# Optimization experiments

Hardware: AMD Instinct MI355X
Metric: run time of the kernel (lower is better)

Reference implementation:

```python
import jax, jax.numpy as jnp
import numpy as np

N, K, F, W = 32768, 32, 4, 256

def setup_inputs() -> dict:
    key = jax.random.key(0)
    ks = jax.random.split(key, 12)
    init = lambda k, shape, fan_in: jax.random.normal(k, shape, jnp.float32) / np.sqrt(fan_in)
    return {
        "h_center": jax.random.normal(ks[0], (N, W), jnp.float32),
        "h_neighbors": jax.random.normal(ks[1], (N, K, W), jnp.float32),
        "differences": jax.random.normal(ks[2], (N, K, F), jnp.float32),
        # filter MLP (depth=2): Dense(W) -> silu -> Dense(W)
        "W_f1": init(ks[3], (F, W), F),
        "b_f1": jnp.zeros((W,), jnp.float32),
        "W_f2": init(ks[4], (W, W), W),
        "b_f2": jnp.zeros((W,), jnp.float32),
        # neighbor projection Dense(W)
        "W_nb": init(ks[5], (W, W), W),
        "b_nb": jnp.zeros((W,), jnp.float32),
        # center projection Dense(W)
        "W_c": init(ks[6], (W, W), W),
        "b_c": jnp.zeros((W,), jnp.float32),
    }

def reference(h_center, h_neighbors, differences, W_f1, b_f1, W_f2, b_f2, W_nb, b_nb, W_c, b_c):
    # filter MLP over edge (difference) features: [N,K,F] -> [N,K,W]
    f = jax.nn.silu(differences @ W_f1 + b_f1)
    filter_kernel = f @ W_f2 + b_f2
    # project neighbor features: [N,K,W]
    h_nb = h_neighbors @ W_nb + b_nb
    # gated message, sum over neighbor axis -> [N,W]
    msg = jnp.sum(filter_kernel * h_nb, axis=-2)
    # center dense + message, silu
    h_out = jax.nn.silu(h_center @ W_c + b_c + msg)
    return h_out
```

## Files before the change

kernel.cpp:

```cpp
#include <hip/hip_runtime.h>
#include <hip/hip_bf16.h>
#include <stdint.h>

#define NN 32768
#define KNBR 32
#define FDIM 4
#define WDIM 256

typedef __attribute__((ext_vector_type(8))) short short8;
typedef __attribute__((ext_vector_type(4))) float f32x4;

__device__ __forceinline__ unsigned int f2bf(float x) {
    union { float f; unsigned int u; } c; c.f = x;
    return (c.u + 0x7FFFu + ((c.u >> 16) & 1u)) >> 16;
}
__device__ __forceinline__ unsigned int pk2(float a, float b) {
    return f2bf(a) | (f2bf(b) << 16);
}
__device__ __forceinline__ float silu_f(float x) {
    return x / (1.0f + __expf(-x));
}

__global__ void prep_weights(const float* __restrict__ Wf2,
                             const float* __restrict__ Wnb,
                             const float* __restrict__ Wc,
                             uint4* __restrict__ ws_out) {
    int t = blockIdx.x * 256 + threadIdx.x;
    int w = t >> 13;
    int q = t & 8191;
    int kt = q >> 10;
    int nt = (q >> 6) & 15;
    int lane = q & 63;
    int k0 = kt * 32 + ((lane >> 4) << 3);
    int col = nt * 16 + (lane & 15);
    const float* src = (w == 0) ? Wf2 : (w == 1) ? Wnb : Wc;
    const float* p = src + (size_t)k0 * 256 + col;
    uint4 o;
    o.x = pk2(p[0],        p[256]);
    o.y = pk2(p[512],      p[768]);
    o.z = pk2(p[1024],     p[1280]);
    o.w = pk2(p[1536],     p[1792]);
    ws_out[t] = o;
}

__global__ __launch_bounds__(512) void msg_kernel(
        const float* __restrict__ nbr,
        const float* __restrict__ diff,
        const float* __restrict__ Wf1,
        const float* __restrict__ b1,
        const float* __restrict__ b2,
        const float* __restrict__ bnb,
        const uint4* __restrict__ wf2_g,
        const uint4* __restrict__ wnb_g,
        float* __restrict__ msg_out)
{
    __shared__ unsigned short f_frag[8 * 8 * 64 * 8];
    __shared__ unsigned short e_frag[8 * 2 * 64 * 8];
    __shared__ unsigned short wnb_s[2 * 16 * 64 * 8];
    __shared__ unsigned short wf2_s[2 * 16 * 64 * 8];
    __shared__ float wf1_s[4 * 256];
    __shared__ float b1_s[256];

    const int tid  = threadIdx.x;
    const int lane = tid & 63;
    const int wid  = tid >> 6;
    const int wm   = wid >> 2;
    const int wn   = wid & 3;
    const int eblk = blockIdx.x * 128;

    for (int i = tid; i < 1024; i += 512) wf1_s[i] = Wf1[i];
    if (tid < 256) b1_s[tid] = b1[tid];
    __syncthreads();

    uint4* ff4 = (uint4*)f_frag;
    #pragma unroll
    for (int j = 0; j < 8; ++j) {
        int q   = tid + j * 512;
        int lq  = q & 63;
        int ktf = (q >> 6) & 7;
        int mt  = q >> 9;
        int row = mt * 16 + (lq & 15);
        int k0  = ktf * 32 + ((lq >> 4) << 3);
        const float4 d4 = *(const float4*)(diff + (size_t)(eblk + row) * 4);
        float vals[8];
        #pragma unroll
        for (int i = 0; i < 8; ++i) {
            int k = k0 + i;
            float v = b1_s[k] + d4.x * wf1_s[k]       + d4.y * wf1_s[256 + k]
                              + d4.z * wf1_s[512 + k] + d4.w * wf1_s[768 + k];
            vals[i] = silu_f(v);
        }
        uint4 o;
        o.x = pk2(vals[0], vals[1]); o.y = pk2(vals[2], vals[3]);
        o.z = pk2(vals[4], vals[5]); o.w = pk2(vals[6], vals[7]);
        ff4[q] = o;
    }
    __syncthreads();

    f32x4 accH[4][4], accP[4][4];
    #pragma unroll
    for (int mt = 0; mt < 4; ++mt)
        #pragma unroll
        for (int nt = 0; nt < 4; ++nt) {
            accH[mt][nt] = (f32x4){0.f, 0.f, 0.f, 0.f};
            accP[mt][nt] = (f32x4){0.f, 0.f, 0.f, 0.f};
        }

    uint4* ef4 = (uint4*)e_frag;
    for (int kt2 = 0; kt2 < 4; ++kt2) {
        {
            int row = tid >> 2, quarter = tid & 3;
            const float* src = nbr + (size_t)(eblk + row) * 256 + kt2 * 64 + quarter * 16;
            float4 v0 = *(const float4*)(src + 0);
            float4 v1 = *(const float4*)(src + 4);
            float4 v2 = *(const float4*)(src + 8);
            float4 v3 = *(const float4*)(src + 12);
            uint4 p0, p1;
            p0.x = pk2(v0.x, v0.y); p0.y = pk2(v0.z, v0.w);
            p0.z = pk2(v1.x, v1.y); p0.w = pk2(v1.z, v1.w);
            p1.x = pk2(v2.x, v2.y); p1.y = pk2(v2.z, v2.w);
            p1.z = pk2(v3.x, v3.y); p1.w = pk2(v3.z, v3.w);
            int mt = row >> 4, kti = quarter >> 1, fr = row & 15;
            int g0 = (quarter & 1) * 2;
            ef4[(mt * 2 + kti) * 64 + g0 * 16 + fr]       = p0;
            ef4[(mt * 2 + kti) * 64 + (g0 + 1) * 16 + fr] = p1;
        }
        {
            const uint4* srcn = wnb_g + kt2 * 2048;
            const uint4* srcf = wf2_g + kt2 * 2048;
            uint4* dn = (uint4*)wnb_s;
            uint4* df = (uint4*)wf2_s;
            #pragma unroll
            for (int j = 0; j < 4; ++j) {
                dn[j * 512 + tid] = srcn[j * 512 + tid];
                df[j * 512 + tid] = srcf[j * 512 + tid];
            }
        }
        __syncthreads();

        #pragma unroll
        for (int kti = 0; kti < 2; ++kti) {
            short8 bN[4], bF[4];
            #pragma unroll
            for (int nt = 0; nt < 4; ++nt) {
                int ntg = wn * 4 + nt;
                bN[nt] = *(const short8*)&wnb_s[((kti * 16 + ntg) * 64 + lane) * 8];
                bF[nt] = *(const short8*)&wf2_s[((kti * 16 + ntg) * 64 + lane) * 8];
            }
            #pragma unroll
            for (int mt = 0; mt < 4; ++mt) {
                int mtg = wm * 4 + mt;
                short8 aE = *(const short8*)&e_frag[((mtg * 2 + kti) * 64 + lane) * 8];
                short8 aF = *(const short8*)&f_frag[((mtg * 8 + kt2 * 2 + kti) * 64 + lane) * 8];
                #pragma unroll
                for (int nt = 0; nt < 4; ++nt) {
                    accH[mt][nt] = __builtin_amdgcn_mfma_f32_16x16x32_bf16(aE, bN[nt], accH[mt][nt], 0, 0, 0);
                    accP[mt][nt] = __builtin_amdgcn_mfma_f32_16x16x32_bf16(aF, bF[nt], accP[mt][nt], 0, 0, 0);
                }
            }
        }
        __syncthreads();
    }

    #pragma unroll
    for (int nd = 0; nd < 2; ++nd) {
        int node = blockIdx.x * 4 + wm * 2 + nd;
        #pragma unroll
        for (int nt = 0; nt < 4; ++nt) {
            int col = wn * 64 + nt * 16 + (lane & 15);
            float vb2 = b2[col];
            float vbn = bnb[col];
            float s = 0.f;
            #pragma unroll
            for (int m2 = 0; m2 < 2; ++m2) {
                int mt = nd * 2 + m2;
                #pragma unroll
                for (int r = 0; r < 4; ++r)
                    s += (accP[mt][nt][r] + vb2) * (accH[mt][nt][r] + vbn);
            }
            s += __shfl_xor(s, 16);
            s += __shfl_xor(s, 32);
            if (lane < 16) msg_out[(size_t)node * 256 + col] = s;
        }
    }
}

__global__ __launch_bounds__(256) void out_kernel(
        const float* __restrict__ hc,
        const float* __restrict__ bc,
        const uint4* __restrict__ wc_g,
        float* __restrict__ out)
{
    __shared__ unsigned short a_s[4 * 2 * 64 * 8];
    __shared__ unsigned short wc_s[2 * 16 * 64 * 8];

    const int tid  = threadIdx.x;
    const int lane = tid & 63;
    const int wn   = tid >> 6;
    const int rblk = blockIdx.x * 64;

    f32x4 acc[4][4];
    #pragma unroll
    for (int mt = 0; mt < 4; ++mt)
        #pragma unroll
        for (int nt = 0; nt < 4; ++nt)
            acc[mt][nt] = (f32x4){0.f, 0.f, 0.f, 0.f};

    uint4* af4 = (uint4*)a_s;
    for (int kt2 = 0; kt2 < 4; ++kt2) {
        {
            int row = tid >> 2, quarter = tid & 3;
            const float* src = hc + (size_t)(rblk + row) * 256 + kt2 * 64 + quarter * 16;
            float4 v0 = *(const float4*)(src + 0);
            float4 v1 = *(const float4*)(src + 4);
            float4 v2 = *(const float4*)(src + 8);
            float4 v3 = *(const float4*)(src + 12);
            uint4 p0, p1;
            p0.x = pk2(v0.x, v0.y); p0.y = pk2(v0.z, v0.w);
            p0.z = pk2(v1.x, v1.y); p0.w = pk2(v1.z, v1.w);
            p1.x = pk2(v2.x, v2.y); p1.y = pk2(v2.z, v2.w);
            p1.z = pk2(v3.x, v3.y); p1.w = pk2(v3.z, v3.w);
            int mt = row >> 4, kti = quarter >> 1, fr = row & 15;
            int g0 = (quarter & 1) * 2;
            af4[(mt * 2 + kti) * 64 + g0 * 16 + fr]       = p0;
            af4[(mt * 2 + kti) * 64 + (g0 + 1) * 16 + fr] = p1;
            const uint4* srcw = wc_g + kt2 * 2048;
            uint4* dw = (uint4*)wc_s;
            #pragma unroll
            for (int j = 0; j < 8; ++j)
                dw[j * 256 + tid] = srcw[j * 256 + tid];
        }
        __syncthreads();
        #pragma unroll
        for (int kti = 0; kti < 2; ++kti) {
            short8 b[4];
            #pragma unroll
            for (int nt = 0; nt < 4; ++nt)
                b[nt] = *(const short8*)&wc_s[((kti * 16 + wn * 4 + nt) * 64 + lane) * 8];
            #pragma unroll
            for (int mt = 0; mt < 4; ++mt) {
                short8 a = *(const short8*)&a_s[((mt * 2 + kti) * 64 + lane) * 8];
                #pragma unroll
                for (int nt = 0; nt < 4; ++nt)
                    acc[mt][nt] = __builtin_amdgcn_mfma_f32_16x16x32_bf16(a, b[nt], acc[mt][nt], 0, 0, 0);
            }
        }
        __syncthreads();
    }

    #pragma unroll
    for (int mt = 0; mt < 4; ++mt)
        #pragma unroll
        for (int nt = 0; nt < 4; ++nt)
            #pragma unroll
            for (int r = 0; r < 4; ++r) {
                int grow = rblk + mt * 16 + ((lane >> 4) << 2) + r;
                int col  = wn * 64 + nt * 16 + (lane & 15);
                size_t idx = (size_t)grow * 256 + col;
                float v = acc[mt][nt][r] + bc[col] + out[idx];
                out[idx] = silu_f(v);
            }
}

extern "C" void kernel_launch(void* const* d_in, const int* in_sizes, int n_in,
                              void* d_out, int out_size, void* d_ws, size_t ws_size,
                              hipStream_t stream) {
    const float* h_center    = (const float*)d_in[0];
    const float* h_neighbors = (const float*)d_in[1];
    const float* differences = (const float*)d_in[2];
    const float* W_f1        = (const float*)d_in[3];
    const float* b_f1        = (const float*)d_in[4];
    const float* W_f2        = (const float*)d_in[5];
    const float* b_f2        = (const float*)d_in[6];
    const float* W_nb        = (const float*)d_in[7];
    const float* b_nb        = (const float*)d_in[8];
    const float* W_c         = (const float*)d_in[9];
    const float* b_c         = (const float*)d_in[10];
    float* out = (float*)d_out;

    uint4* ws4 = (uint4*)d_ws;
    const uint4* wf2_ws = ws4;
    const uint4* wnb_ws = ws4 + 8192;
    const uint4* wc_ws  = ws4 + 16384;

    prep_weights<<<96, 256, 0, stream>>>(W_f2, W_nb, W_c, ws4);
    msg_kernel<<<NN / 4, 512, 0, stream>>>(h_neighbors, differences, W_f1, b_f1,
                                           b_f2, b_nb, wf2_ws, wnb_ws, out);
    out_kernel<<<NN / 64, 256, 0, stream>>>(h_center, b_c, wc_ws, out);
}
```

Before: 713.2 us.

## Split msg kernel into two sequential GEMM phases to cut registers and LDS

Restructures msg_kernel so each block handles 64 edges (2 nodes) and runs the filter GEMM and neighbor-projection GEMM sequentially rather than interleaved. The filter result is stashed in LDS as bf16 (phi_s), which halves the accumulators per wave and drops the large f_frag buffer. Launch bounds now request 4 blocks per CU for higher occupancy. The cost is twice as many blocks, extra barriers, weight tiles reloaded per block for half the edges, and an additional bf16 rounding of the filter output.

```diff
diff --git a/kernel.cpp b/kernel.cpp
--- a/kernel.cpp
+++ b/kernel.cpp
@@ -43,7 +43,7 @@
     ws_out[t] = o;
 }
 
-__global__ __launch_bounds__(512) void msg_kernel(
+__global__ __launch_bounds__(512, 4) void msg_kernel(
         const float* __restrict__ nbr,
         const float* __restrict__ diff,
         const float* __restrict__ Wf1,
@@ -54,109 +54,114 @@
         const uint4* __restrict__ wnb_g,
         float* __restrict__ msg_out)
 {
-    __shared__ unsigned short f_frag[8 * 8 * 64 * 8];
-    __shared__ unsigned short e_frag[8 * 2 * 64 * 8];
-    __shared__ unsigned short wnb_s[2 * 16 * 64 * 8];
-    __shared__ unsigned short wf2_s[2 * 16 * 64 * 8];
-    __shared__ float wf1_s[4 * 256];
+    __shared__ unsigned short stage_s[8 * 64 * 8];
+    __shared__ unsigned short w_s[2 * 16 * 64 * 8];
+    __shared__ unsigned int   phi_s[8192];
+    __shared__ float wf1_s[1024];
     __shared__ float b1_s[256];
 
     const int tid  = threadIdx.x;
     const int lane = tid & 63;
     const int wid  = tid >> 6;
-    const int wm   = wid >> 2;
-    const int wn   = wid & 3;
-    const int eblk = blockIdx.x * 128;
+    const int eblk = blockIdx.x * 64;
+
+    const int g    = wid;
+    const int row  = ((g >> 1) << 4) + (lane & 15);
+    const int klo  = ((g & 1) << 5) + ((lane >> 4) << 3);
 
     for (int i = tid; i < 1024; i += 512) wf1_s[i] = Wf1[i];
     if (tid < 256) b1_s[tid] = b1[tid];
+    const float4 d4 = *(const float4*)(diff + (size_t)(eblk + row) * 4);
+
+    uint4* stage4 = (uint4*)stage_s;
+    uint4* ws4l   = (uint4*)w_s;
+
+    f32x4 acc[4][2];
+    #pragma unroll
+    for (int mt = 0; mt < 4; ++mt) {
+        acc[mt][0] = (f32x4){0.f, 0.f, 0.f, 0.f};
+        acc[mt][1] = (f32x4){0.f, 0.f, 0.f, 0.f};
+    }
+
     __syncthreads();
 
-    uint4* ff4 = (uint4*)f_frag;
-    #pragma unroll
-    for (int j = 0; j < 8; ++j) {
-        int q   = tid + j * 512;
-        int lq  = q & 63;
-        int ktf = (q >> 6) & 7;
-        int mt  = q >> 9;
-        int row = mt * 16 + (lq & 15);
-        int k0  = ktf * 32 + ((lq >> 4) << 3);
-        const float4 d4 = *(const float4*)(diff + (size_t)(eblk + row) * 4);
-        float vals[8];
-        #pragma unroll
-        for (int i = 0; i < 8; ++i) {
-            int k = k0 + i;
-            float v = b1_s[k] + d4.x * wf1_s[k]       + d4.y * wf1_s[256 + k]
-                              + d4.z * wf1_s[512 + k] + d4.w * wf1_s[768 + k];
-            vals[i] = silu_f(v);
-        }
-        uint4 o;
-        o.x = pk2(vals[0], vals[1]); o.y = pk2(vals[2], vals[3]);
-        o.z = pk2(vals[4], vals[5]); o.w = pk2(vals[6], vals[7]);
-        ff4[q] = o;
-    }
-    __syncthreads();
-
-    f32x4 accH[4][4], accP[4][4];
-    #pragma unroll
-    for (int mt = 0; mt < 4; ++mt)
-        #pragma unroll
-        for (int nt = 0; nt < 4; ++nt) {
-            accH[mt][nt] = (f32x4){0.f, 0.f, 0.f, 0.f};
-            accP[mt][nt] = (f32x4){0.f, 0.f, 0.f, 0.f};
-        }
-
-    uint4* ef4 = (uint4*)e_frag;
     for (int kt2 = 0; kt2 < 4; ++kt2) {
         {
-            int row = tid >> 2, quarter = tid & 3;
-            const float* src = nbr + (size_t)(eblk + row) * 256 + kt2 * 64 + quarter * 16;
-            float4 v0 = *(const float4*)(src + 0);
+            const int kb = kt2 * 64 + klo;
+            float vals[8];
+            #pragma unroll
+            for (int i = 0; i < 8; ++i) {
+                int k = kb + i;
+                float v = b1_s[k] + d4.x * wf1_s[k]       + d4.y * wf1_s[256 + k]
+                                  + d4.z * wf1_s[512 + k] + d4.w * wf1_s[768 + k];
+                vals[i] = silu_f(v);
+            }
+            uint4 o;
+            o.x = pk2(vals[0], vals[1]); o.y = pk2(vals[2], vals[3]);
+            o.z = pk2(vals[4], vals[5]); o.w = pk2(vals[6], vals[7]);
+            stage4[tid] = o;
+        }
+        {
+            const uint4* srcw = wf2_g + (size_t)kt2 * 2048;
+            ws4l[tid]        = srcw[tid];
+            ws4l[512 + tid]  = srcw[512 + tid];
+            ws4l[1024 + tid] = srcw[1024 + tid];
+            ws4l[1536 + tid] = srcw[1536 + tid];
+        }
+        __syncthreads();
+        #pragma unroll
+        for (int kti = 0; kti < 2; ++kti) {
+            short8 bA = *(const short8*)&w_s[((kti * 16 + wid * 2 + 0) * 64 + lane) * 8];
+            short8 bB = *(const short8*)&w_s[((kti * 16 + wid * 2 + 1) * 64 + lane) * 8];
+            #pragma unroll
+            for (int mt = 0; mt < 4; ++mt) {
+                short8 a = *(const short8*)&stage_s[((mt * 2 + kti) * 64 + lane) * 8];
+                acc[mt][0] = __builtin_amdgcn_mfma_f32_16x16x32_bf16(a, bA, acc[mt][0], 0, 0, 0);
+                acc[mt][1] = __builtin_amdgcn_mfma_f32_16x16x32_bf16(a, bB, acc[mt][1], 0, 0, 0);
+            }
+        }
+        __syncthreads();
+    }
+
+    #pragma unroll
+    for (int nt = 0; nt < 2; ++nt) {
+        float vb2 = b2[wid * 32 + nt * 16 + (lane & 15)];
+        #pragma unroll
+        for (int mt = 0; mt < 4; ++mt) {
+            int base = (((wid * 2 + nt) * 4 + mt) * 64 + lane) * 2;
+            phi_s[base]     = pk2(acc[mt][nt][0] + vb2, acc[mt][nt][1] + vb2);
+            phi_s[base + 1] = pk2(acc[mt][nt][2] + vb2, acc[mt][nt][3] + vb2);
+            acc[mt][nt] = (f32x4){0.f, 0.f, 0.f, 0.f};
+        }
+    }
+
+    for (int kt2 = 0; kt2 < 4; ++kt2) {
+        {
+            const float* src = nbr + (size_t)(eblk + row) * 256 + kt2 * 64 + klo;
+            float4 v0 = *(const float4*)(src);
             float4 v1 = *(const float4*)(src + 4);
-            float4 v2 = *(const float4*)(src + 8);
-            float4 v3 = *(const float4*)(src + 12);
-            uint4 p0, p1;
-            p0.x = pk2(v0.x, v0.y); p0.y = pk2(v0.z, v0.w);
-            p0.z = pk2(v1.x, v1.y); p0.w = pk2(v1.z, v1.w);
-            p1.x = pk2(v2.x, v2.y); p1.y = pk2(v2.z, v2.w);
-            p1.z = pk2(v3.x, v3.y); p1.w = pk2(v3.z, v3.w);
-            int mt = row >> 4, kti = quarter >> 1, fr = row & 15;
-            int g0 = (quarter & 1) * 2;
-            ef4[(mt * 2 + kti) * 64 + g0 * 16 + fr]       = p0;
-            ef4[(mt * 2 + kti) * 64 + (g0 + 1) * 16 + fr] = p1;
-        }
-        {
-            const uint4* srcn = wnb_g + kt2 * 2048;
-            const uint4* srcf = wf2_g + kt2 * 2048;
-            uint4* dn = (uint4*)wnb_s;
-            uint4* df = (uint4*)wf2_s;
-            #pragma unroll
-            for (int j = 0; j < 4; ++j) {
-                dn[j * 512 + tid] = srcn[j * 512 + tid];
-                df[j * 512 + tid] = srcf[j * 512 + tid];
-            }
-        }
-        __syncthreads();
-
+            uint4 o;
+            o.x = pk2(v0.x, v0.y); o.y = pk2(v0.z, v0.w);
+            o.z = pk2(v1.x, v1.y); o.w = pk2(v1.z, v1.w);
+            stage4[tid] = o;
+        }
+        {
+            const uint4* srcw = wnb_g + (size_t)kt2 * 2048;
+            ws4l[tid]        = srcw[tid];
+            ws4l[512 + tid]  = srcw[512 + tid];
+            ws4l[1024 + tid] = srcw[1024 + tid];
+            ws4l[1536 + tid] = srcw[1536 + tid];
+        }
+        __syncthreads();
         #pragma unroll
         for (int kti = 0; kti < 2; ++kti) {
-            short8 bN[4], bF[4];
-            #pragma unroll
-            for (int nt = 0; nt < 4; ++nt) {
-                int ntg = wn * 4 + nt;
-                bN[nt] = *(const short8*)&wnb_s[((kti * 16 + ntg) * 64 + lane) * 8];
-                bF[nt] = *(const short8*)&wf2_s[((kti * 16 + ntg) * 64 + lane) * 8];
-            }
+            short8 bA = *(const short8*)&w_s[((kti * 16 + wid * 2 + 0) * 64 + lane) * 8];
+            short8 bB = *(const short8*)&w_s[((kti * 16 + wid * 2 + 1) * 64 + lane) * 8];
             #pragma unroll
             for (int mt = 0; mt < 4; ++mt) {
-                int mtg = wm * 4 + mt;
-                short8 aE = *(const short8*)&e_frag[((mtg * 2 + kti) * 64 + lane) * 8];
-                short8 aF = *(const short8*)&f_frag[((mtg * 8 + kt2 * 2 + kti) * 64 + lane) * 8];
-                #pragma unroll
-                for (int nt = 0; nt < 4; ++nt) {
-                    accH[mt][nt] = __builtin_amdgcn_mfma_f32_16x16x32_bf16(aE, bN[nt], accH[mt][nt], 0, 0, 0);
-                    accP[mt][nt] = __builtin_amdgcn_mfma_f32_16x16x32_bf16(aF, bF[nt], accP[mt][nt], 0, 0, 0);
-                }
+                short8 a = *(const short8*)&stage_s[((mt * 2 + kti) * 64 + lane) * 8];
+                acc[mt][0] = __builtin_amdgcn_mfma_f32_16x16x32_bf16(a, bA, acc[mt][0], 0, 0, 0);
+                acc[mt][1] = __builtin_amdgcn_mfma_f32_16x16x32_bf16(a, bB, acc[mt][1], 0, 0, 0);
             }
         }
         __syncthreads();
@@ -164,19 +169,23 @@
 
     #pragma unroll
     for (int nd = 0; nd < 2; ++nd) {
-        int node = blockIdx.x * 4 + wm * 2 + nd;
-        #pragma unroll
-        for (int nt = 0; nt < 4; ++nt) {
-            int col = wn * 64 + nt * 16 + (lane & 15);
-            float vb2 = b2[col];
-            float vbn = bnb[col];
+        int node = blockIdx.x * 2 + nd;
+        #pragma unroll
+        for (int nt = 0; nt < 2; ++nt) {
+            int col = wid * 32 + nt * 16 + (lane & 15);
+            float bn = bnb[col];
             float s = 0.f;
             #pragma unroll
             for (int m2 = 0; m2 < 2; ++m2) {
                 int mt = nd * 2 + m2;
-                #pragma unroll
-                for (int r = 0; r < 4; ++r)
-                    s += (accP[mt][nt][r] + vb2) * (accH[mt][nt][r] + vbn);
+                int base = (((wid * 2 + nt) * 4 + mt) * 64 + lane) * 2;
+                unsigned int p01 = phi_s[base], p23 = phi_s[base + 1];
+                float ph0 = __uint_as_float(p01 << 16);
+                float ph1 = __uint_as_float(p01 & 0xffff0000u);
+                float ph2 = __uint_as_float(p23 << 16);
+                float ph3 = __uint_as_float(p23 & 0xffff0000u);
+                s += ph0 * (acc[mt][nt][0] + bn) + ph1 * (acc[mt][nt][1] + bn)
+                   + ph2 * (acc[mt][nt][2] + bn) + ph3 * (acc[mt][nt][3] + bn);
             }
             s += __shfl_xor(s, 16);
             s += __shfl_xor(s, 32);
@@ -284,7 +293,7 @@
     const uint4* wc_ws  = ws4 + 16384;
 
     prep_weights<<<96, 256, 0, stream>>>(W_f2, W_nb, W_c, ws4);
-    msg_kernel<<<NN / 4, 512, 0, stream>>>(h_neighbors, differences, W_f1, b_f1,
+    msg_kernel<<<NN / 2, 512, 0, stream>>>(h_neighbors, differences, W_f1, b_f1,
                                            b_f2, b_nb, wf2_ws, wnb_ws, out);
     out_kernel<<<NN / 64, 256, 0, stream>>>(h_center, b_c, wc_ws, out);
 }
```

New measurement: 640.0 us. 1.11x faster.

## Make msg kernel persistent over tiles with register-resident weights and double buffering

Applied to the files above, without the earlier changes.

Rewrites the message kernel so that each block processes 8 tiles of 64 edges. The W_f2 and W_nb fragments are loaded once into registers per wave, instead of being restaged through shared memory on every k-step. The next tile's neighbor and difference loads are issued before the current tile's MFMAs, and the converted fragments are written to a double-buffered LDS slot, so global latency overlaps with compute. A cheaper round-to-nearest bf16 pack is also used. The large register footprint (64 short8 weight fragments) with launch_bounds(512,2) risks spilling or low occupancy.

```diff
diff --git a/kernel.cpp b/kernel.cpp
--- a/kernel.cpp
+++ b/kernel.cpp
@@ -6,6 +6,7 @@
 #define KNBR 32
 #define FDIM 4
 #define WDIM 256
+#define TPB_TILES 8
 
 typedef __attribute__((ext_vector_type(8))) short short8;
 typedef __attribute__((ext_vector_type(4))) float f32x4;
@@ -16,6 +17,11 @@
 }
 __device__ __forceinline__ unsigned int pk2(float a, float b) {
     return f2bf(a) | (f2bf(b) << 16);
+}
+__device__ __forceinline__ unsigned int pkr(float a, float b) {
+    unsigned ua = __float_as_uint(a) + 0x8000u;
+    unsigned ub = __float_as_uint(b) + 0x8000u;
+    return (ua >> 16) | (ub & 0xFFFF0000u);
 }
 __device__ __forceinline__ float silu_f(float x) {
     return x / (1.0f + __expf(-x));
@@ -43,7 +49,7 @@
     ws_out[t] = o;
 }
 
-__global__ __launch_bounds__(512) void msg_kernel(
+__global__ __launch_bounds__(512, 2) void msg_kernel(
         const float* __restrict__ nbr,
         const float* __restrict__ diff,
         const float* __restrict__ Wf1,
@@ -54,134 +60,178 @@
         const uint4* __restrict__ wnb_g,
         float* __restrict__ msg_out)
 {
-    __shared__ unsigned short f_frag[8 * 8 * 64 * 8];
-    __shared__ unsigned short e_frag[8 * 2 * 64 * 8];
-    __shared__ unsigned short wnb_s[2 * 16 * 64 * 8];
-    __shared__ unsigned short wf2_s[2 * 16 * 64 * 8];
-    __shared__ float wf1_s[4 * 256];
+    __shared__ uint4 fbuf[2][2048];
+    __shared__ uint4 ebuf[2][2048];
+    __shared__ float wf1_s[1024];
     __shared__ float b1_s[256];
 
     const int tid  = threadIdx.x;
     const int lane = tid & 63;
     const int wid  = tid >> 6;
-    const int wm   = wid >> 2;
-    const int wn   = wid & 3;
-    const int eblk = blockIdx.x * 128;
+    const int srow = tid >> 3;
+    const int skti = tid & 7;
+    const int smt  = srow >> 4;
+    const int sfr  = srow & 15;
+    const int mtf  = lane >> 4;
+    const int frf  = lane & 15;
 
     for (int i = tid; i < 1024; i += 512) wf1_s[i] = Wf1[i];
     if (tid < 256) b1_s[tid] = b1[tid];
+
+    const short8* wf2p = (const short8*)wf2_g;
+    const short8* wnbp = (const short8*)wnb_g;
+    short8 bF[8][2], bN[8][2];
+    #pragma unroll
+    for (int kti = 0; kti < 8; ++kti) {
+        #pragma unroll
+        for (int nt = 0; nt < 2; ++nt) {
+            const int idx = (kti * 16 + wid * 2 + nt) * 64 + lane;
+            bF[kti][nt] = wf2p[idx];
+            bN[kti][nt] = wnbp[idx];
+        }
+    }
+    float vb2[2], vbn[2];
+    #pragma unroll
+    for (int nt = 0; nt < 2; ++nt) {
+        const int col = wid * 32 + nt * 16 + frf;
+        vb2[nt] = b2[col];
+        vbn[nt] = bnb[col];
+    }
+
+    f32x4 accP[4][2], accH[4][2];
+    #pragma unroll
+    for (int mt = 0; mt < 4; ++mt)
+        #pragma unroll
+        for (int nt = 0; nt < 2; ++nt) {
+            accP[mt][nt] = (f32x4){0.f,0.f,0.f,0.f};
+            accH[mt][nt] = (f32x4){0.f,0.f,0.f,0.f};
+        }
+
+    const int tbase = blockIdx.x * TPB_TILES;
+
+    auto stage_f = [&](int bsel, float4 d4) {
+        uint4* fb = fbuf[bsel];
+        const float4* w4 = (const float4*)wf1_s;
+        const float4* b4 = (const float4*)b1_s;
+        #pragma unroll
+        for (int g = 0; g < 4; ++g) {
+            const int o = wid * 8 + g * 2;
+            float4 ba = b4[o],      bb = b4[o+1];
+            float4 w0a = w4[o],     w0b = w4[o+1];
+            float4 w1a = w4[64+o],  w1b = w4[64+o+1];
+            float4 w2a = w4[128+o], w2b = w4[128+o+1];
+            float4 w3a = w4[192+o], w3b = w4[192+o+1];
+            float v0 = silu_f(ba.x + d4.x*w0a.x + d4.y*w1a.x + d4.z*w2a.x + d4.w*w3a.x);
+            float v1 = silu_f(ba.y + d4.x*w0a.y + d4.y*w1a.y + d4.z*w2a.y + d4.w*w3a.y);
+            float v2 = silu_f(ba.z + d4.x*w0a.z + d4.y*w1a.z + d4.z*w2a.z + d4.w*w3a.z);
+            float v3 = silu_f(ba.w + d4.x*w0a.w + d4.y*w1a.w + d4.z*w2a.w + d4.w*w3a.w);
+            float v4 = silu_f(bb.x + d4.x*w0b.x + d4.y*w1b.x + d4.z*w2b.x + d4.w*w3b.x);
+            float v5 = silu_f(bb.y + d4.x*w0b.y + d4.y*w1b.y + d4.z*w2b.y + d4.w*w3b.y);
+            float v6 = silu_f(bb.z + d4.x*w0b.z + d4.y*w1b.z + d4.z*w2b.z + d4.w*w3b.z);
+            float v7 = silu_f(bb.w + d4.x*w0b.w + d4.y*w1b.w + d4.z*w2b.w + d4.w*w3b.w);
+            uint4 o4;
+            o4.x = pkr(v0, v1); o4.y = pkr(v2, v3);
+            o4.z = pkr(v4, v5); o4.w = pkr(v6, v7);
+            fb[(mtf * 8 + wid) * 64 + g * 16 + frf] = o4;
+        }
+    };
+    auto stage_e = [&](int bsel, const float4* evA, const float4* evB) {
+        uint4* eb = ebuf[bsel];
+        #pragma unroll
+        for (int g = 0; g < 2; ++g) {
+            float4 a = evA[g*2], b = evA[g*2+1];
+            uint4 o4;
+            o4.x = pkr(a.x,a.y); o4.y = pkr(a.z,a.w);
+            o4.z = pkr(b.x,b.y); o4.w = pkr(b.z,b.w);
+            eb[(smt * 8 + skti) * 64 + g * 16 + sfr] = o4;
+        }
+        #pragma unroll
+        for (int g = 2; g < 4; ++g) {
+            float4 a = evB[(g-2)*2], b = evB[(g-2)*2+1];
+            uint4 o4;
+            o4.x = pkr(a.x,a.y); o4.y = pkr(a.z,a.w);
+            o4.z = pkr(b.x,b.y); o4.w = pkr(b.z,b.w);
+            eb[(smt * 8 + skti) * 64 + g * 16 + sfr] = o4;
+        }
+    };
+
     __syncthreads();
 
-    uint4* ff4 = (uint4*)f_frag;
-    #pragma unroll
-    for (int j = 0; j < 8; ++j) {
-        int q   = tid + j * 512;
-        int lq  = q & 63;
-        int ktf = (q >> 6) & 7;
-        int mt  = q >> 9;
-        int row = mt * 16 + (lq & 15);
-        int k0  = ktf * 32 + ((lq >> 4) << 3);
-        const float4 d4 = *(const float4*)(diff + (size_t)(eblk + row) * 4);
-        float vals[8];
-        #pragma unroll
-        for (int i = 0; i < 8; ++i) {
-            int k = k0 + i;
-            float v = b1_s[k] + d4.x * wf1_s[k]       + d4.y * wf1_s[256 + k]
-                              + d4.z * wf1_s[512 + k] + d4.w * wf1_s[768 + k];
-            vals[i] = silu_f(v);
-        }
-        uint4 o;
-        o.x = pk2(vals[0], vals[1]); o.y = pk2(vals[2], vals[3]);
-        o.z = pk2(vals[4], vals[5]); o.w = pk2(vals[6], vals[7]);
-        ff4[q] = o;
+    {
+        const int eblk = tbase * 64;
+        float4 d4 = *(const float4*)(diff + (size_t)(eblk + lane) * 4);
+        const float4* ep = (const float4*)(nbr + (size_t)(eblk + srow) * 256 + skti * 32);
+        float4 evA[4] = {ep[0], ep[1], ep[2], ep[3]};
+        float4 evB[4] = {ep[4], ep[5], ep[6], ep[7]};
+        stage_e(0, evA, evB);
+        stage_f(0, d4);
     }
     __syncthreads();
 
-    f32x4 accH[4][4], accP[4][4];
-    #pragma unroll
-    for (int mt = 0; mt < 4; ++mt)
-        #pragma unroll
-        for (int nt = 0; nt < 4; ++nt) {
-            accH[mt][nt] = (f32x4){0.f, 0.f, 0.f, 0.f};
-            accP[mt][nt] = (f32x4){0.f, 0.f, 0.f, 0.f};
-        }
-
-    uint4* ef4 = (uint4*)e_frag;
-    for (int kt2 = 0; kt2 < 4; ++kt2) {
+    for (int t = 0; t < TPB_TILES; ++t) {
+        const int cur = t & 1;
+        const bool more = (t + 1 < TPB_TILES);
+
+        float4 d4n = (float4){0.f,0.f,0.f,0.f};
+        float4 evA[4], evB[4];
+        if (more) {
+            const int eblk = (tbase + t + 1) * 64;
+            d4n = *(const float4*)(diff + (size_t)(eblk + lane) * 4);
+            const float4* epn = (const float4*)(nbr + (size_t)(eblk + srow) * 256 + skti * 32);
+            evA[0] = epn[0]; evA[1] = epn[1]; evA[2] = epn[2]; evA[3] = epn[3];
+            evB[0] = epn[4]; evB[1] = epn[5]; evB[2] = epn[6]; evB[3] = epn[7];
+        }
+
         {
-            int row = tid >> 2, quarter = tid & 3;
-            const float* src = nbr + (size_t)(eblk + row) * 256 + kt2 * 64 + quarter * 16;
-            float4 v0 = *(const float4*)(src + 0);
-            float4 v1 = *(const float4*)(src + 4);
-            float4 v2 = *(const float4*)(src + 8);
-            float4 v3 = *(const float4*)(src + 12);
-            uint4 p0, p1;
-            p0.x = pk2(v0.x, v0.y); p0.y = pk2(v0.z, v0.w);
-            p0.z = pk2(v1.x, v1.y); p0.w = pk2(v1.z, v1.w);
-            p1.x = pk2(v2.x, v2.y); p1.y = pk2(v2.z, v2.w);
-            p1.z = pk2(v3.x, v3.y); p1.w = pk2(v3.z, v3.w);
-            int mt = row >> 4, kti = quarter >> 1, fr = row & 15;
-            int g0 = (quarter & 1) * 2;
-            ef4[(mt * 2 + kti) * 64 + g0 * 16 + fr]       = p0;
-            ef4[(mt * 2 + kti) * 64 + (g0 + 1) * 16 + fr] = p1;
-        }
-        {
-            const uint4* srcn = wnb_g + kt2 * 2048;
-            const uint4* srcf = wf2_g + kt2 * 2048;
-            uint4* dn = (uint4*)wnb_s;
-            uint4* df = (uint4*)wf2_s;
-            #pragma unroll
-            for (int j = 0; j < 4; ++j) {
-                dn[j * 512 + tid] = srcn[j * 512 + tid];
-                df[j * 512 + tid] = srcf[j * 512 + tid];
-            }
-        }
+            const short8* fb = (const short8*)fbuf[cur];
+            const short8* eb = (const short8*)ebuf[cur];
+            #pragma unroll
+            for (int kti = 0; kti < 8; ++kti) {
+                #pragma unroll
+                for (int mt = 0; mt < 4; ++mt) {
+                    short8 aF = fb[(mt * 8 + kti) * 64 + lane];
+                    short8 aE = eb[(mt * 8 + kti) * 64 + lane];
+                    accP[mt][0] = __builtin_amdgcn_mfma_f32_16x16x32_bf16(aF, bF[kti][0], accP[mt][0], 0, 0, 0);
+                    accP[mt][1] = __builtin_amdgcn_mfma_f32_16x16x32_bf16(aF, bF[kti][1], accP[mt][1], 0, 0, 0);
+                    accH[mt][0] = __builtin_amdgcn_mfma_f32_16x16x32_bf16(aE, bN[kti][0], accH[mt][0], 0, 0, 0);
+                    accH[mt][1] = __builtin_amdgcn_mfma_f32_16x16x32_bf16(aE, bN[kti][1], accH[mt][1], 0, 0, 0);
+                }
+            }
+        }
+
+        if (more) {
+            stage_e(1 - cur, evA, evB);
+            stage_f(1 - cur, d4n);
+        }
+
+        const int nodeBase = (tbase + t) * 2;
+        #pragma unroll
+        for (int nd = 0; nd < 2; ++nd) {
+            #pragma unroll
+            for (int nt = 0; nt < 2; ++nt) {
+                float s = 0.f;
+                #pragma unroll
+                for (int m2 = 0; m2 < 2; ++m2) {
+                    const int mt = nd * 2 + m2;
+                    #pragma unroll
+                    for (int r = 0; r < 4; ++r)
+                        s += (accP[mt][nt][r] + vb2[nt]) * (accH[mt][nt][r] + vbn[nt]);
+                }
+                s += __shfl_xor(s, 16);
+                s += __shfl_xor(s, 32);
+                if (lane < 16)
+                    msg_out[(size_t)(nodeBase + nd) * 256 + wid * 32 + nt * 16 + lane] = s;
+            }
+        }
+        #pragma unroll
+        for (int mt = 0; mt < 4; ++mt)
+            #pragma unroll
+            for (int nt = 0; nt < 2; ++nt) {
+                accP[mt][nt] = (f32x4){0.f,0.f,0.f,0.f};
+                accH[mt][nt] = (f32x4){0.f,0.f,0.f,0.f};
+            }
+
         __syncthreads();
-
-        #pragma unroll
-        for (int kti = 0; kti < 2; ++kti) {
-            short8 bN[4], bF[4];
-            #pragma unroll
-            for (int nt = 0; nt < 4; ++nt) {
-                int ntg = wn * 4 + nt;
-                bN[nt] = *(const short8*)&wnb_s[((kti * 16 + ntg) * 64 + lane) * 8];
-                bF[nt] = *(const short8*)&wf2_s[((kti * 16 + ntg) * 64 + lane) * 8];
-            }
-            #pragma unroll
-            for (int mt = 0; mt < 4; ++mt) {
-                int mtg = wm * 4 + mt;
-                short8 aE = *(const short8*)&e_frag[((mtg * 2 + kti) * 64 + lane) * 8];
-                short8 aF = *(const short8*)&f_frag[((mtg * 8 + kt2 * 2 + kti) * 64 + lane) * 8];
-                #pragma unroll
-                for (int nt = 0; nt < 4; ++nt) {
-                    accH[mt][nt] = __builtin_amdgcn_mfma_f32_16x16x32_bf16(aE, bN[nt], accH[mt][nt], 0, 0, 0);
-                    accP[mt][nt] = __builtin_amdgcn_mfma_f32_16x16x32_bf16(aF, bF[nt], accP[mt][nt], 0, 0, 0);
-                }
-            }
-        }
-        __syncthreads();
-    }
-
-    #pragma unroll
-    for (int nd = 0; nd < 2; ++nd) {
-        int node = blockIdx.x * 4 + wm * 2 + nd;
-        #pragma unroll
-        for (int nt = 0; nt < 4; ++nt) {
-            int col = wn * 64 + nt * 16 + (lane & 15);
-            float vb2 = b2[col];
-            float vbn = bnb[col];
-            float s = 0.f;
-            #pragma unroll
-            for (int m2 = 0; m2 < 2; ++m2) {
-                int mt = nd * 2 + m2;
-                #pragma unroll
-                for (int r = 0; r < 4; ++r)
-                    s += (accP[mt][nt][r] + vb2) * (accH[mt][nt][r] + vbn);
-            }
-            s += __shfl_xor(s, 16);
-            s += __shfl_xor(s, 32);
-            if (lane < 16) msg_out[(size_t)node * 256 + col] = s;
-        }
     }
 }
 
@@ -284,7 +334,7 @@
     const uint4* wc_ws  = ws4 + 16384;
 
     prep_weights<<<96, 256, 0, stream>>>(W_f2, W_nb, W_c, ws4);
-    msg_kernel<<<NN / 4, 512, 0, stream>>>(h_neighbors, differences, W_f1, b_f1,
-                                           b_f2, b_nb, wf2_ws, wnb_ws, out);
+    msg_kernel<<<NN / 2 / TPB_TILES, 512, 0, stream>>>(
+        h_neighbors, differences, W_f1, b_f1, b_f2, b_nb, wf2_ws, wnb_ws, out);
     out_kernel<<<NN / 64, 256, 0, stream>>>(h_center, b_c, wc_ws, out);
 }
```

Result: slower. 845.7 us (+18.6%).
